# Kernel optimization log

Measured on AMD Instinct MI355X. Metric: run time of the kernel, lower is better.

## Reference

```python
import jax, jax.numpy as jnp
import numpy as np

B, L, D, N = 2, 2048, 1024, 16
DT_MIN, DT_MAX = 1e-3, 1e-1


def setup_inputs() -> dict:
    key = jax.random.key(0)
    ks = jax.random.split(key, 8)
    u = jax.random.normal(ks[0], (B, L, D), dtype=jnp.float32)
    # torch.nn.Linear weights are (out_features, in_features)
    W_dt = jax.random.normal(ks[1], (D, D), dtype=jnp.float32) * 0.02
    b_dt = jnp.zeros((D,), dtype=jnp.float32)
    W_B = jax.random.normal(ks[2], (D * N, D), dtype=jnp.float32) * 0.02
    b_B = jnp.zeros((D * N,), dtype=jnp.float32)
    W_C = jax.random.normal(ks[3], (D * N, D), dtype=jnp.float32) * 0.02
    b_C = jnp.zeros((D * N,), dtype=jnp.float32)
    # log_A init: log(1..N) broadcast over channels (HiPPO-ish diagonal)
    log_A = jnp.broadcast_to(jnp.log(jnp.arange(1, N + 1, dtype=jnp.float32)), (D, N))
    D_skip = jnp.ones((D,), dtype=jnp.float32)
    lo, hi = float(np.log(DT_MIN)), float(np.log(DT_MAX))
    dt_bias = jax.random.uniform(ks[4], (D,), dtype=jnp.float32) * (hi - lo) + lo
    return {"u": u, "log_A": log_A, "D_skip": D_skip, "dt_bias": dt_bias,
            "W_dt": W_dt, "b_dt": b_dt, "W_B": W_B, "b_B": b_B,
            "W_C": W_C, "b_C": b_C}


def reference(u, log_A, D_skip, dt_bias, W_dt, b_dt, W_B, b_B, W_C, b_C):
    b, l, d = u.shape
    n = log_A.shape[1]
    A = -jnp.exp(log_A)                                   # (d, n), A < 0
    # token-dependent parameters, computed for all timesteps at once
    dt = jax.nn.softplus(u @ W_dt.T + b_dt + dt_bias)     # (b, l, d)
    Bt = (u @ W_B.T + b_B).reshape(b, l, d, n)            # (b, l, d, n)
    Ct = (u @ W_C.T + b_C).reshape(b, l, d, n)            # (b, l, d, n)
    # exact ZOH discretisation
    A_bar = jnp.exp(dt[..., None] * A)                    # (b, l, d, n)
    B_bar = (A_bar - 1.0) / A * Bt                        # (b, l, d, n)
    x_in = B_bar * u[..., None]                           # (b, l, d, n)
    # recurrent scan over time
    def step(h, inp):
        a_t, x_t, c_t = inp                               # each (b, d, n)
        h = a_t * h + x_t
        y_t = jnp.sum(c_t * h, axis=-1)                   # (b, d)
        return h, y_t
    h0 = jnp.zeros((b, d, n), dtype=u.dtype)
    xs = (jnp.moveaxis(A_bar, 1, 0), jnp.moveaxis(x_in, 1, 0), jnp.moveaxis(Ct, 1, 0))
    _, ys = jax.lax.scan(step, h0, xs)                    # ys: (l, b, d)
    y = jnp.moveaxis(ys, 0, 1) + D_skip * u               # (b, l, d)
    return y
```

## Files before the change

### kernel.cpp

```cpp
#include <hip/hip_runtime.h>
#include <hip/hip_bf16.h>
#include <stdint.h>

constexpr int Bb = 2;
constexpr int Ll = 2048;
constexpr int Dd = 1024;
constexpr int Nn = 16;
constexpr int NB = Dd * Nn;
constexpr int SL = 64;
constexpr int NCH = Bb * Dd;
constexpr int KCAT = 3 * Dd;

typedef __bf16 bf16_t;
typedef __bf16 bf16x8 __attribute__((ext_vector_type(8)));
typedef __bf16 bf16x4 __attribute__((ext_vector_type(4)));
typedef float f32x4 __attribute__((ext_vector_type(4)));

__device__ inline void gld_lds16(const void* g, void* l) {
    __builtin_amdgcn_global_load_lds(
        (const __attribute__((address_space(1))) unsigned int*)g,
        (__attribute__((address_space(3))) unsigned int*)l, 16, 0, 0);
}

__global__ __launch_bounds__(256) void cvt_bf16(const float* __restrict__ s,
                                                bf16_t* __restrict__ d, int n4) {
    int i = blockIdx.x * 256 + threadIdx.x;
    const int stride = gridDim.x * 256;
    const float4* s4 = (const float4*)s;
    bf16x4* d4 = (bf16x4*)d;
    for (; i < n4; i += stride) {
        float4 v = s4[i];
        bf16x4 o = {(bf16_t)v.x, (bf16_t)v.y, (bf16_t)v.z, (bf16_t)v.w};
        d4[i] = o;
    }
}

__global__ __launch_bounds__(256) void build_ucat(const float* __restrict__ u,
                                                  bf16_t* __restrict__ ucat) {
    const int i = blockIdx.x * 256 + threadIdx.x;
    const int row = i >> 8;
    const int c = (i & 255) << 2;
    float4 v = ((const float4*)u)[i];
    bf16x4 hi = {(bf16_t)v.x, (bf16_t)v.y, (bf16_t)v.z, (bf16_t)v.w};
    bf16x4 lo = {(bf16_t)(v.x - (float)hi.x), (bf16_t)(v.y - (float)hi.y),
                 (bf16_t)(v.z - (float)hi.z), (bf16_t)(v.w - (float)hi.w)};
    bf16_t* r = ucat + (size_t)row * KCAT;
    *(bf16x4*)(r + c) = hi;
    *(bf16x4*)(r + Dd + c) = lo;
    *(bf16x4*)(r + 2 * Dd + c) = hi;
}

__global__ __launch_bounds__(256) void build_wcat(const float* __restrict__ w,
                                                  bf16_t* __restrict__ wcat) {
    const int i = blockIdx.x * 256 + threadIdx.x;
    const int row = i >> 8;
    const int c = (i & 255) << 2;
    float4 v = ((const float4*)w)[i];
    bf16x4 hi = {(bf16_t)v.x, (bf16_t)v.y, (bf16_t)v.z, (bf16_t)v.w};
    bf16x4 lo = {(bf16_t)(v.x - (float)hi.x), (bf16_t)(v.y - (float)hi.y),
                 (bf16_t)(v.z - (float)hi.z), (bf16_t)(v.w - (float)hi.w)};
    bf16_t* r = wcat + (size_t)row * KCAT;
    *(bf16x4*)(r + c) = hi;
    *(bf16x4*)(r + Dd + c) = hi;
    *(bf16x4*)(r + 2 * Dd + c) = lo;
}

template <int EP, typename OutT>
__global__ __launch_bounds__(256) void gemm_mfma(
    const bf16_t* __restrict__ Abase, int CL, int l0, int K,
    const bf16_t* __restrict__ W, const float* __restrict__ b1,
    const float* __restrict__ b2, OutT* __restrict__ C, int N)
{
    __shared__ bf16_t As[128 * 32];
    __shared__ bf16_t Bs[128 * 32];

    const int tid = threadIdx.x;
    const int bn = blockIdx.x * 128;
    const int rglob = blockIdx.y * 128;
    const int batch = rglob / CL;
    const int rin = rglob % CL;
    const bf16_t* Ap = Abase + ((size_t)batch * Ll + l0 + rin) * K;
    const bf16_t* Wp = W + (size_t)bn * K;
    OutT* Cp = C + (size_t)rglob * N;

    const int sr = tid >> 2;
    const int sc = (tid & 3) << 3;
    char* ldsA = (char*)As + tid * 16;
    char* ldsB = (char*)Bs + tid * 16;

    const int lane = tid & 63;
    const int wid = tid >> 6;
    const int wm = (wid & 1) << 6;
    const int wn = (wid >> 1) << 6;
    const int lr = lane & 15;
    const int lq = lane >> 4;

    f32x4 acc[4][4] = {};

    for (int k0 = 0; k0 < K; k0 += 32) {
        __syncthreads();
        gld_lds16(Ap + (size_t)sr * K + k0 + sc, ldsA);
        gld_lds16(Ap + (size_t)(sr + 64) * K + k0 + sc, ldsA + 4096);
        gld_lds16(Wp + (size_t)sr * K + k0 + sc, ldsB);
        gld_lds16(Wp + (size_t)(sr + 64) * K + k0 + sc, ldsB + 4096);
        __syncthreads();

        bf16x8 af[4], bfr[4];
#pragma unroll
        for (int mi = 0; mi < 4; ++mi)
            af[mi] = *(const bf16x8*)&As[(wm + mi * 16 + lr) * 32 + lq * 8];
#pragma unroll
        for (int ni = 0; ni < 4; ++ni)
            bfr[ni] = *(const bf16x8*)&Bs[(wn + ni * 16 + lr) * 32 + lq * 8];
#pragma unroll
        for (int mi = 0; mi < 4; ++mi)
#pragma unroll
            for (int ni = 0; ni < 4; ++ni)
                acc[mi][ni] = __builtin_amdgcn_mfma_f32_16x16x32_bf16(
                    af[mi], bfr[ni], acc[mi][ni], 0, 0, 0);
    }

#pragma unroll
    for (int ni = 0; ni < 4; ++ni) {
        const int col = bn + wn + ni * 16 + lr;
        const float bc = b1[col] + (EP == 1 ? b2[col] : 0.f);
#pragma unroll
        for (int mi = 0; mi < 4; ++mi)
#pragma unroll
            for (int i = 0; i < 4; ++i) {
                float v = acc[mi][ni][i] + bc;
                if (EP == 1) v = (v > 20.f) ? v : log1pf(__expf(v));
                Cp[(size_t)(wm + mi * 16 + lq * 4 + i) * N + col] = (OutT)v;
            }
    }
}

__global__ __launch_bounds__(256) void gemm_dt(
    const bf16_t* __restrict__ A, int K, const bf16_t* __restrict__ W,
    const float* __restrict__ b1, const float* __restrict__ b2,
    float* __restrict__ C)
{
    __shared__ bf16_t As[128 * 32];
    __shared__ bf16_t Bs[64 * 32];

    const int tid = threadIdx.x;
    const int bn = blockIdx.x * 64;
    const int row0 = blockIdx.y * 128;
    const bf16_t* Ap = A + (size_t)row0 * K;
    const bf16_t* Wp = W + (size_t)bn * K;
    float* Cp = C + (size_t)row0 * Dd;

    const int sr = tid >> 2;
    const int sc = (tid & 3) << 3;
    char* ldsA = (char*)As + tid * 16;
    char* ldsB = (char*)Bs + tid * 16;

    const int lane = tid & 63;
    const int wid = tid >> 6;
    const int wm = (wid & 1) << 6;
    const int wn = (wid >> 1) << 5;
    const int lr = lane & 15;
    const int lq = lane >> 4;

    f32x4 acc[4][2] = {};

    for (int k0 = 0; k0 < K; k0 += 32) {
        __syncthreads();
        gld_lds16(Ap + (size_t)sr * K + k0 + sc, ldsA);
        gld_lds16(Ap + (size_t)(sr + 64) * K + k0 + sc, ldsA + 4096);
        gld_lds16(Wp + (size_t)sr * K + k0 + sc, ldsB);
        __syncthreads();

        bf16x8 af[4], bfr[2];
#pragma unroll
        for (int mi = 0; mi < 4; ++mi)
            af[mi] = *(const bf16x8*)&As[(wm + mi * 16 + lr) * 32 + lq * 8];
#pragma unroll
        for (int ni = 0; ni < 2; ++ni)
            bfr[ni] = *(const bf16x8*)&Bs[(wn + ni * 16 + lr) * 32 + lq * 8];
#pragma unroll
        for (int mi = 0; mi < 4; ++mi)
#pragma unroll
            for (int ni = 0; ni < 2; ++ni)
                acc[mi][ni] = __builtin_amdgcn_mfma_f32_16x16x32_bf16(
                    bfr[ni], af[mi], acc[mi][ni], 0, 0, 0);
    }

#pragma unroll
    for (int ni = 0; ni < 2; ++ni) {
        const int col = bn + wn + ni * 16 + lq * 4;
        const float4 ba = *(const float4*)&b1[col];
        const float4 bb = *(const float4*)&b2[col];
        const float bc[4] = {ba.x + bb.x, ba.y + bb.y, ba.z + bb.z, ba.w + bb.w};
#pragma unroll
        for (int mi = 0; mi < 4; ++mi) {
            const int row = wm + mi * 16 + lr;
            f32x4 v;
#pragma unroll
            for (int i = 0; i < 4; ++i) {
                float t = acc[mi][ni][i] + bc[i];
                v[i] = (t > 20.f) ? t : log1pf(__expf(t));
            }
            *(f32x4*)(Cp + (size_t)row * Dd + col) = v;
        }
    }
}

__global__ __launch_bounds__(512, 2) void gemm256_bc(
    const bf16_t* __restrict__ Abase, int CL, int l0, int K,
    const bf16_t* __restrict__ WB, const bf16_t* __restrict__ WC,
    const float* __restrict__ bB, const float* __restrict__ bC,
    bf16_t* __restrict__ OB, bf16_t* __restrict__ OC)
{
    extern __shared__ char smem[];
    const int tid = threadIdx.x;

    const int NY = (2 * CL) >> 8;
    const int id = blockIdx.x;
    const int cx = id & 7;
    const int jj = id >> 3;
    const int x = cx * 16 + jj / NY;
    const int yb = jj % NY;

    const int rglob = yb * 256;
    const int batch = rglob / CL;
    const int rin = rglob % CL;
    const bf16_t* Ap = Abase + ((size_t)batch * Ll + l0 + rin) * K;

    const bf16_t* Wp; const float* bias; bf16_t* Co; int bn;
    if (x < 64) { Wp = WB; bias = bB; Co = OB; bn = x * 256; }
    else        { Wp = WC; bias = bC; Co = OC; bn = (x - 64) * 256; }
    Wp += (size_t)bn * K;
    bf16_t* Cp = Co + (size_t)rglob * NB;

    const int lane = tid & 63;
    const int wid = tid >> 6;
    const int wr = wid >> 2;
    const int wc = wid & 3;
    const int lr = lane & 15;
    const int lq = lane >> 4;
    const int NT = K >> 6;

    const int c0 = tid, c1 = tid + 512;
    const int r0 = c0 >> 3, r1 = c1 >> 3;
    const int kb0 = ((c0 & 7) << 3) ^ ((r0 & 7) << 3);
    const int kb1 = ((c1 & 7) << 3) ^ ((r1 & 7) << 3);

    auto stage = [&](const bf16_t* src, char* dst, int tt, int h) {
        gld_lds16(src + (size_t)(h * 128 + r0) * K + tt * 64 + kb0,
                  dst + h * 16384 + c0 * 16);
        gld_lds16(src + (size_t)(h * 128 + r1) * K + tt * 64 + kb1,
                  dst + h * 16384 + c1 * 16);
    };

    stage(Ap, smem, 0, 0);
    stage(Ap, smem, 0, 1);
    stage(Wp, smem + 32768, 0, 0);
    stage(Wp, smem + 32768, 0, 1);
    if (NT > 1) {
        stage(Wp, smem + 65536 + 32768, 1, 0);
        stage(Wp, smem + 65536 + 32768, 1, 1);
        asm volatile("s_waitcnt vmcnt(4)" ::: "memory");
    } else {
        asm volatile("s_waitcnt vmcnt(0)" ::: "memory");
    }
    __builtin_amdgcn_s_barrier();

    f32x4 acc[8][4] = {};
    const int xsw = (lr & 7) << 4;

    for (int t = 0; t < NT; ++t) {
        char* Ard = smem + ((t & 1) ? 65536 : 0);
        char* Brd = Ard + 32768;
        char* Awr = smem + ((t & 1) ? 0 : 65536);
        char* Bwr = Brd;

        bf16x8 bfr[2][4];
#pragma unroll
        for (int p = 0; p < 4; ++p) {
            if (p == 0) { if (t + 1 < NT) stage(Ap, Awr, t + 1, 0); }
            if (p == 1) { if (t + 1 < NT) stage(Ap, Awr, t + 1, 1); }
            if (p == 2) { if (t + 2 < NT) stage(Wp, Bwr, t + 2, 0); }
            if (p == 3) { if (t + 2 < NT) stage(Wp, Bwr, t + 2, 1); }

            if (p == 0) {
#pragma unroll
                for (int ks = 0; ks < 2; ++ks)
#pragma unroll
                    for (int ni = 0; ni < 4; ++ni)
                        bfr[ks][ni] = *(const bf16x8*)(Brd +
                            (wc * 64 + ni * 16 + lr) * 128 +
                            ((ks * 64 + lq * 16) ^ xsw));
            }
            bf16x8 a0k0 = *(const bf16x8*)(Ard +
                (wr * 128 + (2 * p) * 16 + lr) * 128 + ((lq * 16) ^ xsw));
            bf16x8 a0k1 = *(const bf16x8*)(Ard +
                (wr * 128 + (2 * p) * 16 + lr) * 128 + ((64 + lq * 16) ^ xsw));
            bf16x8 a1k0 = *(const bf16x8*)(Ard +
                (wr * 128 + (2 * p + 1) * 16 + lr) * 128 + ((lq * 16) ^ xsw));
            bf16x8 a1k1 = *(const bf16x8*)(Ard +
                (wr * 128 + (2 * p + 1) * 16 + lr) * 128 + ((64 + lq * 16) ^ xsw));

            __builtin_amdgcn_s_barrier();
            __builtin_amdgcn_s_setprio(1);
#pragma unroll
            for (int ni = 0; ni < 4; ++ni) {
                acc[2 * p][ni] = __builtin_amdgcn_mfma_f32_16x16x32_bf16(
                    bfr[0][ni], a0k0, acc[2 * p][ni], 0, 0, 0);
                acc[2 * p][ni] = __builtin_amdgcn_mfma_f32_16x16x32_bf16(
                    bfr[1][ni], a0k1, acc[2 * p][ni], 0, 0, 0);
                acc[2 * p + 1][ni] = __builtin_amdgcn_mfma_f32_16x16x32_bf16(
                    bfr[0][ni], a1k0, acc[2 * p + 1][ni], 0, 0, 0);
                acc[2 * p + 1][ni] = __builtin_amdgcn_mfma_f32_16x16x32_bf16(
                    bfr[1][ni], a1k1, acc[2 * p + 1][ni], 0, 0, 0);
            }
            __builtin_amdgcn_s_setprio(0);
            if (p == 3) {
                if (t + 2 < NT)
                    asm volatile("s_waitcnt vmcnt(4)" ::: "memory");
                else if (t + 1 < NT)
                    asm volatile("s_waitcnt vmcnt(0)" ::: "memory");
            }
            __builtin_amdgcn_s_barrier();
        }
    }

    float4 bv[4];
#pragma unroll
    for (int ni = 0; ni < 4; ++ni)
        bv[ni] = *(const float4*)&bias[bn + wc * 64 + ni * 16 + lq * 4];
#pragma unroll
    for (int mi = 0; mi < 8; ++mi) {
        const size_t rowoff = (size_t)(wr * 128 + mi * 16 + lr) * NB;
#pragma unroll
        for (int ni = 0; ni < 4; ++ni) {
            const int col = bn + wc * 64 + ni * 16 + lq * 4;
            bf16x4 o = {(bf16_t)(acc[mi][ni][0] + bv[ni].x),
                        (bf16_t)(acc[mi][ni][1] + bv[ni].y),
                        (bf16_t)(acc[mi][ni][2] + bv[ni].z),
                        (bf16_t)(acc[mi][ni][3] + bv[ni].w)};
            *(bf16x4*)(Cp + rowoff + col) = o;
        }
    }
}

__global__ __launch_bounds__(256) void scan_seg_local(
    const float* __restrict__ u, const float* __restrict__ dt,
    const bf16_t* __restrict__ Bt_c, const float* __restrict__ log_A,
    float* __restrict__ pseg, float* __restrict__ hseg, int CL, int l0)
{
    const int tid = threadIdx.x;
    const int g = tid >> 4, n = tid & 15;
    const int gid = blockIdx.x * 16 + g;
    const int ch = gid & (NCH - 1);
    const int s = gid >> 11;
    const int b = ch >> 10, d = ch & (Dd - 1);

    const float A = -__expf(log_A[d * Nn + n]);
    const float rA = 1.f / A;

    size_t idx_bn = (size_t)(b * CL + s * SL) * NB + d * Nn + n;
    size_t idx_u = ((size_t)b * Ll + l0 + s * SL) * Dd + d;

    float p = 1.f, h = 0.f;
    for (int l = 0; l < SL; ++l) {
        const float dtv = dt[idx_u];
        const float uv = u[idx_u];
        const float bv = (float)Bt_c[idx_bn];
        const float a = __expf(dtv * A);
        p *= a;
        h = a * h + (a - 1.f) * rA * bv * uv;
        idx_bn += NB; idx_u += Dd;
    }
    const size_t o = ((size_t)s * NCH + ch) * Nn + n;
    pseg[o] = p;
    hseg[o] = h;
}

__global__ __launch_bounds__(256) void scan_combine(
    const float* __restrict__ pseg, const float* __restrict__ hseg,
    float* __restrict__ hin_arr, float* __restrict__ h_state,
    int NSEG, int l0)
{
    const int t = blockIdx.x * 256 + threadIdx.x;
    float hin = (l0 == 0) ? 0.f : h_state[t];
    for (int s = 0; s < NSEG; ++s) {
        const size_t o = (size_t)s * (NCH * Nn) + t;
        hin_arr[o] = hin;
        hin = pseg[o] * hin + hseg[o];
    }
    h_state[t] = hin;
}

__global__ __launch_bounds__(256) void scan_seg_final(
    const float* __restrict__ u, const float* __restrict__ dt,
    const bf16_t* __restrict__ Bt_c, const bf16_t* __restrict__ Ct_c,
    const float* __restrict__ log_A, const float* __restrict__ D_skip,
    const float* __restrict__ hin_arr, float* __restrict__ y, int CL, int l0)
{
    const int tid = threadIdx.x;
    const int g = tid >> 4, n = tid & 15;
    const int gid = blockIdx.x * 16 + g;
    const int ch = gid & (NCH - 1);
    const int s = gid >> 11;
    const int b = ch >> 10, d = ch & (Dd - 1);

    const float A = -__expf(log_A[d * Nn + n]);
    const float rA = 1.f / A;
    const float Dsk = D_skip[d];

    size_t idx_bn = (size_t)(b * CL + s * SL) * NB + d * Nn + n;
    size_t idx_u = ((size_t)b * Ll + l0 + s * SL) * Dd + d;

    float h = hin_arr[((size_t)s * NCH + ch) * Nn + n];
    for (int l = 0; l < SL; ++l) {
        const float dtv = dt[idx_u];
        const float uv = u[idx_u];
        const float bv = (float)Bt_c[idx_bn];
        const float cv = (float)Ct_c[idx_bn];
        const float a = __expf(dtv * A);
        h = a * h + (a - 1.f) * rA * bv * uv;
        float p = cv * h;
        p += __shfl_xor(p, 1);
        p += __shfl_xor(p, 2);
        p += __shfl_xor(p, 4);
        p += __shfl_xor(p, 8);
        if (n == 0) y[idx_u] = p + Dsk * uv;
        idx_bn += NB; idx_u += Dd;
    }
}

static inline size_t al256(size_t x) { return (x + 255) & ~(size_t)255; }

extern "C" void kernel_launch(void* const* d_in, const int* in_sizes, int n_in,
                              void* d_out, int out_size, void* d_ws, size_t ws_size,
                              hipStream_t stream) {
    const float* u       = (const float*)d_in[0];
    const float* log_A   = (const float*)d_in[1];
    const float* D_skip  = (const float*)d_in[2];
    const float* dt_bias = (const float*)d_in[3];
    const float* W_dt    = (const float*)d_in[4];
    const float* b_dt    = (const float*)d_in[5];
    const float* W_B     = (const float*)d_in[6];
    const float* b_B     = (const float*)d_in[7];
    const float* W_C     = (const float*)d_in[8];
    const float* b_C     = (const float*)d_in[9];
    float* y = (float*)d_out;

    hipFuncSetAttribute(reinterpret_cast<const void*>(gemm256_bc),
                        hipFuncAttributeMaxDynamicSharedMemorySize, 131072);

    const size_t sz_ubf  = al256((size_t)Bb * Ll * Dd * 2);
    const size_t sz_w    = al256((size_t)NB * Dd * 2);
    const size_t sz_h    = al256((size_t)NCH * Nn * 4);
    const size_t sz_dtf  = al256((size_t)Bb * Ll * Dd * 4);
    const size_t sz_ucat = al256((size_t)Bb * Ll * KCAT * 2);
    const size_t sz_wcat = al256((size_t)Dd * KCAT * 2);

    int CL = 128;
    const int cands[5] = {2048, 1024, 512, 256, 128};
    for (int i = 0; i < 5; ++i) {
        const int c = cands[i];
        const int nseg = c / SL;
        const size_t seg = 3 * al256((size_t)nseg * NCH * Nn * 4);
        const size_t chunk = 2 * al256((size_t)2 * c * NB * 2);
        const size_t ovl = sz_ucat + sz_wcat;
        const size_t need = sz_ubf + 2 * sz_w + sz_h + sz_dtf + seg +
                            (chunk > ovl ? chunk : ovl);
        if (need <= ws_size) { CL = c; break; }
    }
    const int NSEG = CL / SL;

    char* p = (char*)d_ws;
    bf16_t* u_bf   = (bf16_t*)p; p += sz_ubf;
    bf16_t* wB_bf  = (bf16_t*)p; p += sz_w;
    bf16_t* wC_bf  = (bf16_t*)p; p += sz_w;
    float* h_state = (float*)p; p += sz_h;
    float* dt_full = (float*)p; p += sz_dtf;
    const size_t sz_seg1 = al256((size_t)NSEG * NCH * Nn * 4);
    float* pseg    = (float*)p; p += sz_seg1;
    float* hseg    = (float*)p; p += sz_seg1;
    float* hin_arr = (float*)p; p += sz_seg1;
    char* chunk0 = p;
    bf16_t* Bt_c = (bf16_t*)chunk0;
    bf16_t* Ct_c = (bf16_t*)(chunk0 + al256((size_t)2 * CL * NB * 2));
    bf16_t* u_cat = (bf16_t*)chunk0;
    bf16_t* w_cat = (bf16_t*)(chunk0 + sz_ucat);

    cvt_bf16<<<2048, 256, 0, stream>>>(u, u_bf, Bb * Ll * Dd / 4);
    cvt_bf16<<<2048, 256, 0, stream>>>(W_B, wB_bf, NB * Dd / 4);
    cvt_bf16<<<2048, 256, 0, stream>>>(W_C, wC_bf, NB * Dd / 4);
    build_ucat<<<Bb * Ll * Dd / 4 / 256, 256, 0, stream>>>(u, u_cat);
    build_wcat<<<Dd * Dd / 4 / 256, 256, 0, stream>>>(W_dt, w_cat);

    gemm_dt<<<dim3(Dd / 64, Bb * Ll / 128), 256, 0, stream>>>(
        u_cat, KCAT, w_cat, b_dt, dt_bias, dt_full);

    const bool use256 = (CL % 256 == 0);
    for (int l0 = 0; l0 < Ll; l0 += CL) {
        if (use256) {
            const int NY = 2 * CL / 256;
            gemm256_bc<<<dim3(128 * NY), 512, 131072, stream>>>(
                u_bf, CL, l0, Dd, wB_bf, wC_bf, b_B, b_C, Bt_c, Ct_c);
        } else {
            gemm_mfma<0, bf16_t><<<dim3(NB / 128, 2 * CL / 128), 256, 0, stream>>>(
                u_bf, CL, l0, Dd, wB_bf, b_B, nullptr, Bt_c, NB);
            gemm_mfma<0, bf16_t><<<dim3(NB / 128, 2 * CL / 128), 256, 0, stream>>>(
                u_bf, CL, l0, Dd, wC_bf, b_C, nullptr, Ct_c, NB);
        }
        scan_seg_local<<<dim3(128 * NSEG), 256, 0, stream>>>(
            u, dt_full, Bt_c, log_A, pseg, hseg, CL, l0);
        scan_combine<<<dim3(128), 256, 0, stream>>>(
            pseg, hseg, hin_arr, h_state, NSEG, l0);
        scan_seg_final<<<dim3(128 * NSEG), 256, 0, stream>>>(
            u, dt_full, Bt_c, Ct_c, log_A, D_skip, hin_arr, y, CL, l0);
    }
}
```

Measured before the change: 689.1 us.

## Shrink B/C GEMM tile to 256x128 with triple-buffered weights for higher occupancy

```diff
diff --git a/kernel.cpp b/kernel.cpp
--- a/kernel.cpp
+++ b/kernel.cpp
@@ -36,7 +36,8 @@
 }
 
 __global__ __launch_bounds__(256) void build_ucat(const float* __restrict__ u,
-                                                  bf16_t* __restrict__ ucat) {
+                                                  bf16_t* __restrict__ ucat,
+                                                  bf16_t* __restrict__ ubf) {
     const int i = blockIdx.x * 256 + threadIdx.x;
     const int row = i >> 8;
     const int c = (i & 255) << 2;
@@ -48,6 +49,7 @@
     *(bf16x4*)(r + c) = hi;
     *(bf16x4*)(r + Dd + c) = lo;
     *(bf16x4*)(r + 2 * Dd + c) = hi;
+    *(bf16x4*)(ubf + (size_t)i * 4) = hi;
 }
 
 __global__ __launch_bounds__(256) void build_wcat(const float* __restrict__ w,
@@ -206,7 +208,7 @@
     }
 }
 
-__global__ __launch_bounds__(512, 2) void gemm256_bc(
+__global__ __launch_bounds__(512, 4) void gemm256_bc(
     const bf16_t* __restrict__ Abase, int CL, int l0, int K,
     const bf16_t* __restrict__ WB, const bf16_t* __restrict__ WC,
     const float* __restrict__ bB, const float* __restrict__ bC,
@@ -219,7 +221,8 @@
     const int id = blockIdx.x;
     const int cx = id & 7;
     const int jj = id >> 3;
-    const int x = cx * 16 + jj / NY;
+    const int xs_per = (gridDim.x >> 3) / NY;
+    const int x = cx * xs_per + jj / NY;
     const int yb = jj % NY;
 
     const int rglob = yb * 256;
@@ -228,101 +231,80 @@
     const bf16_t* Ap = Abase + ((size_t)batch * Ll + l0 + rin) * K;
 
     const bf16_t* Wp; const float* bias; bf16_t* Co; int bn;
-    if (x < 64) { Wp = WB; bias = bB; Co = OB; bn = x * 256; }
-    else        { Wp = WC; bias = bC; Co = OC; bn = (x - 64) * 256; }
+    if (x < 128) { Wp = WB; bias = bB; Co = OB; bn = x * 128; }
+    else         { Wp = WC; bias = bC; Co = OC; bn = (x - 128) * 128; }
     Wp += (size_t)bn * K;
     bf16_t* Cp = Co + (size_t)rglob * NB;
 
     const int lane = tid & 63;
     const int wid = tid >> 6;
-    const int wr = wid >> 2;
-    const int wc = wid & 3;
+    const int wr = wid >> 1;
+    const int wc = wid & 1;
     const int lr = lane & 15;
     const int lq = lane >> 4;
-    const int NT = K >> 6;
-
-    const int c0 = tid, c1 = tid + 512;
-    const int r0 = c0 >> 3, r1 = c1 >> 3;
-    const int kb0 = ((c0 & 7) << 3) ^ ((r0 & 7) << 3);
-    const int kb1 = ((c1 & 7) << 3) ^ ((r1 & 7) << 3);
-
-    auto stage = [&](const bf16_t* src, char* dst, int tt, int h) {
-        gld_lds16(src + (size_t)(h * 128 + r0) * K + tt * 64 + kb0,
-                  dst + h * 16384 + c0 * 16);
-        gld_lds16(src + (size_t)(h * 128 + r1) * K + tt * 64 + kb1,
-                  dst + h * 16384 + c1 * 16);
+    const int NT = K >> 5;
+
+    const int r0 = tid >> 2;
+    const int ksrc = (((tid & 3) ^ ((r0 >> 1) & 3)) << 3);
+
+    auto stageA = [&](int tt, int h) {
+        gld_lds16(Ap + (size_t)(h * 128 + r0) * K + tt * 32 + ksrc,
+                  smem + (tt & 1) * 16384 + h * 8192 + tid * 16);
     };
-
-    stage(Ap, smem, 0, 0);
-    stage(Ap, smem, 0, 1);
-    stage(Wp, smem + 32768, 0, 0);
-    stage(Wp, smem + 32768, 0, 1);
+    auto stageB = [&](int tt, int slot) {
+        gld_lds16(Wp + (size_t)r0 * K + tt * 32 + ksrc,
+                  smem + 32768 + slot * 8192 + tid * 16);
+    };
+
+    stageA(0, 0); stageA(0, 1);
+    stageB(0, 0);
     if (NT > 1) {
-        stage(Wp, smem + 65536 + 32768, 1, 0);
-        stage(Wp, smem + 65536 + 32768, 1, 1);
-        asm volatile("s_waitcnt vmcnt(4)" ::: "memory");
+        stageB(1, 1);
+        asm volatile("s_waitcnt vmcnt(1)" ::: "memory");
     } else {
         asm volatile("s_waitcnt vmcnt(0)" ::: "memory");
     }
     __builtin_amdgcn_s_barrier();
 
-    f32x4 acc[8][4] = {};
-    const int xsw = (lr & 7) << 4;
+    f32x4 acc[4][4] = {};
+    const int lqx = (lq << 4) ^ (((lr >> 1) & 3) << 4);
+    int bR = 0;
 
     for (int t = 0; t < NT; ++t) {
-        char* Ard = smem + ((t & 1) ? 65536 : 0);
-        char* Brd = Ard + 32768;
-        char* Awr = smem + ((t & 1) ? 0 : 65536);
-        char* Bwr = Brd;
-
-        bf16x8 bfr[2][4];
-#pragma unroll
-        for (int p = 0; p < 4; ++p) {
-            if (p == 0) { if (t + 1 < NT) stage(Ap, Awr, t + 1, 0); }
-            if (p == 1) { if (t + 1 < NT) stage(Ap, Awr, t + 1, 1); }
-            if (p == 2) { if (t + 2 < NT) stage(Wp, Bwr, t + 2, 0); }
-            if (p == 3) { if (t + 2 < NT) stage(Wp, Bwr, t + 2, 1); }
-
-            if (p == 0) {
-#pragma unroll
-                for (int ks = 0; ks < 2; ++ks)
-#pragma unroll
-                    for (int ni = 0; ni < 4; ++ni)
-                        bfr[ks][ni] = *(const bf16x8*)(Brd +
-                            (wc * 64 + ni * 16 + lr) * 128 +
-                            ((ks * 64 + lq * 16) ^ xsw));
-            }
-            bf16x8 a0k0 = *(const bf16x8*)(Ard +
-                (wr * 128 + (2 * p) * 16 + lr) * 128 + ((lq * 16) ^ xsw));
-            bf16x8 a0k1 = *(const bf16x8*)(Ard +
-                (wr * 128 + (2 * p) * 16 + lr) * 128 + ((64 + lq * 16) ^ xsw));
-            bf16x8 a1k0 = *(const bf16x8*)(Ard +
-                (wr * 128 + (2 * p + 1) * 16 + lr) * 128 + ((lq * 16) ^ xsw));
-            bf16x8 a1k1 = *(const bf16x8*)(Ard +
-                (wr * 128 + (2 * p + 1) * 16 + lr) * 128 + ((64 + lq * 16) ^ xsw));
-
-            __builtin_amdgcn_s_barrier();
-            __builtin_amdgcn_s_setprio(1);
-#pragma unroll
-            for (int ni = 0; ni < 4; ++ni) {
-                acc[2 * p][ni] = __builtin_amdgcn_mfma_f32_16x16x32_bf16(
-                    bfr[0][ni], a0k0, acc[2 * p][ni], 0, 0, 0);
-                acc[2 * p][ni] = __builtin_amdgcn_mfma_f32_16x16x32_bf16(
-                    bfr[1][ni], a0k1, acc[2 * p][ni], 0, 0, 0);
-                acc[2 * p + 1][ni] = __builtin_amdgcn_mfma_f32_16x16x32_bf16(
-                    bfr[0][ni], a1k0, acc[2 * p + 1][ni], 0, 0, 0);
-                acc[2 * p + 1][ni] = __builtin_amdgcn_mfma_f32_16x16x32_bf16(
-                    bfr[1][ni], a1k1, acc[2 * p + 1][ni], 0, 0, 0);
-            }
-            __builtin_amdgcn_s_setprio(0);
-            if (p == 3) {
-                if (t + 2 < NT)
-                    asm volatile("s_waitcnt vmcnt(4)" ::: "memory");
-                else if (t + 1 < NT)
-                    asm volatile("s_waitcnt vmcnt(0)" ::: "memory");
-            }
-            __builtin_amdgcn_s_barrier();
+        if (t + 1 < NT) { stageA(t + 1, 0); stageA(t + 1, 1); }
+        int bS = bR + 2; if (bS >= 3) bS -= 3;
+        if (t + 2 < NT) stageB(t + 2, bS);
+
+        const char* Ard = smem + (t & 1) * 16384;
+        const char* Brd = smem + 32768 + bR * 8192;
+        bf16x8 afr[4], bfr[4];
+#pragma unroll
+        for (int mi = 0; mi < 4; ++mi) {
+            const int row = wr * 64 + mi * 16 + lr;
+            afr[mi] = *(const bf16x8*)(Ard + (row >> 7) * 8192 +
+                                       (row & 127) * 64 + lqx);
         }
+#pragma unroll
+        for (int ni = 0; ni < 4; ++ni) {
+            const int row = wc * 64 + ni * 16 + lr;
+            bfr[ni] = *(const bf16x8*)(Brd + row * 64 + lqx);
+        }
+
+        __builtin_amdgcn_s_barrier();
+        __builtin_amdgcn_s_setprio(1);
+#pragma unroll
+        for (int mi = 0; mi < 4; ++mi)
+#pragma unroll
+            for (int ni = 0; ni < 4; ++ni)
+                acc[mi][ni] = __builtin_amdgcn_mfma_f32_16x16x32_bf16(
+                    bfr[ni], afr[mi], acc[mi][ni], 0, 0, 0);
+        __builtin_amdgcn_s_setprio(0);
+        if (t + 2 < NT)
+            asm volatile("s_waitcnt vmcnt(1)" ::: "memory");
+        else if (t + 1 < NT)
+            asm volatile("s_waitcnt vmcnt(0)" ::: "memory");
+        __builtin_amdgcn_s_barrier();
+        bR = bR + 1; if (bR >= 3) bR -= 3;
     }
 
     float4 bv[4];
@@ -330,8 +312,8 @@
     for (int ni = 0; ni < 4; ++ni)
         bv[ni] = *(const float4*)&bias[bn + wc * 64 + ni * 16 + lq * 4];
 #pragma unroll
-    for (int mi = 0; mi < 8; ++mi) {
-        const size_t rowoff = (size_t)(wr * 128 + mi * 16 + lr) * NB;
+    for (int mi = 0; mi < 4; ++mi) {
+        const size_t rowoff = (size_t)(wr * 64 + mi * 16 + lr) * NB;
 #pragma unroll
         for (int ni = 0; ni < 4; ++ni) {
             const int col = bn + wc * 64 + ni * 16 + lq * 4;
@@ -448,7 +430,7 @@
     float* y = (float*)d_out;
 
     hipFuncSetAttribute(reinterpret_cast<const void*>(gemm256_bc),
-                        hipFuncAttributeMaxDynamicSharedMemorySize, 131072);
+                        hipFuncAttributeMaxDynamicSharedMemorySize, 57344);
 
     const size_t sz_ubf  = al256((size_t)Bb * Ll * Dd * 2);
     const size_t sz_w    = al256((size_t)NB * Dd * 2);
@@ -487,10 +469,9 @@
     bf16_t* u_cat = (bf16_t*)chunk0;
     bf16_t* w_cat = (bf16_t*)(chunk0 + sz_ucat);
 
-    cvt_bf16<<<2048, 256, 0, stream>>>(u, u_bf, Bb * Ll * Dd / 4);
     cvt_bf16<<<2048, 256, 0, stream>>>(W_B, wB_bf, NB * Dd / 4);
     cvt_bf16<<<2048, 256, 0, stream>>>(W_C, wC_bf, NB * Dd / 4);
-    build_ucat<<<Bb * Ll * Dd / 4 / 256, 256, 0, stream>>>(u, u_cat);
+    build_ucat<<<Bb * Ll * Dd / 4 / 256, 256, 0, stream>>>(u, u_cat, u_bf);
     build_wcat<<<Dd * Dd / 4 / 256, 256, 0, stream>>>(W_dt, w_cat);
 
     gemm_dt<<<dim3(Dd / 64, Bb * Ll / 128), 256, 0, stream>>>(
@@ -500,7 +481,7 @@
     for (int l0 = 0; l0 < Ll; l0 += CL) {
         if (use256) {
             const int NY = 2 * CL / 256;
-            gemm256_bc<<<dim3(128 * NY), 512, 131072, stream>>>(
+            gemm256_bc<<<dim3(256 * NY), 512, 57344, stream>>>(
                 u_bf, CL, l0, Dd, wB_bf, wC_bf, b_B, b_C, Bt_c, Ct_c);
         } else {
             gemm_mfma<0, bf16_t><<<dim3(NB / 128, 2 * CL / 128), 256, 0, stream>>>(
```

Result: slower. 719.0 us (+4.3%).

## Deepen GEMM prefetch pipelines and fold u bf16 conversion into build_ucat

Applied to the files above, without the earlier changes.

```diff
diff --git a/kernel.cpp b/kernel.cpp
--- a/kernel.cpp
+++ b/kernel.cpp
@@ -36,7 +36,8 @@
 }
 
 __global__ __launch_bounds__(256) void build_ucat(const float* __restrict__ u,
-                                                  bf16_t* __restrict__ ucat) {
+                                                  bf16_t* __restrict__ ucat,
+                                                  bf16_t* __restrict__ ubf) {
     const int i = blockIdx.x * 256 + threadIdx.x;
     const int row = i >> 8;
     const int c = (i & 255) << 2;
@@ -48,6 +49,7 @@
     *(bf16x4*)(r + c) = hi;
     *(bf16x4*)(r + Dd + c) = lo;
     *(bf16x4*)(r + 2 * Dd + c) = hi;
+    *(bf16x4*)(ubf + (size_t)i * 4) = hi;
 }
 
 __global__ __launch_bounds__(256) void build_wcat(const float* __restrict__ w,
@@ -135,71 +137,111 @@
     }
 }
 
-__global__ __launch_bounds__(256) void gemm_dt(
+__global__ __launch_bounds__(512, 4) void gemm_dt(
     const bf16_t* __restrict__ A, int K, const bf16_t* __restrict__ W,
     const float* __restrict__ b1, const float* __restrict__ b2,
     float* __restrict__ C)
 {
-    __shared__ bf16_t As[128 * 32];
-    __shared__ bf16_t Bs[64 * 32];
-
+    extern __shared__ char smem[];
+    char* const smA = smem;
+    char* const smB = smem + 49152;
     const int tid = threadIdx.x;
-    const int bn = blockIdx.x * 64;
+    const int bn = blockIdx.x * 128;
     const int row0 = blockIdx.y * 128;
     const bf16_t* Ap = A + (size_t)row0 * K;
     const bf16_t* Wp = W + (size_t)bn * K;
     float* Cp = C + (size_t)row0 * Dd;
 
-    const int sr = tid >> 2;
-    const int sc = (tid & 3) << 3;
-    char* ldsA = (char*)As + tid * 16;
-    char* ldsB = (char*)Bs + tid * 16;
-
     const int lane = tid & 63;
     const int wid = tid >> 6;
-    const int wm = (wid & 1) << 6;
-    const int wn = (wid >> 1) << 5;
+    const int wr = wid >> 2;
+    const int wc = wid & 3;
     const int lr = lane & 15;
     const int lq = lane >> 4;
+    const int NT = K >> 6;
+
+    const int c0 = tid, c1 = tid + 512;
+    const int r0 = c0 >> 3, r1 = c1 >> 3;
+    const int kb0 = ((c0 & 7) << 3) ^ ((r0 & 7) << 3);
+    const int kb1 = ((c1 & 7) << 3) ^ ((r1 & 7) << 3);
+
+    auto stageA = [&](int tt, int slot) {
+        gld_lds16(Ap + (size_t)r0 * K + tt * 64 + kb0, smA + slot * 16384 + c0 * 16);
+        gld_lds16(Ap + (size_t)r1 * K + tt * 64 + kb1, smA + slot * 16384 + c1 * 16);
+    };
+    auto stageB = [&](int tt, int slot) {
+        gld_lds16(Wp + (size_t)r0 * K + tt * 64 + kb0, smB + slot * 16384 + c0 * 16);
+        gld_lds16(Wp + (size_t)r1 * K + tt * 64 + kb1, smB + slot * 16384 + c1 * 16);
+    };
+
+    stageA(0, 0); stageB(0, 0); stageA(1, 1); stageB(1, 1);
+    asm volatile("s_waitcnt vmcnt(4)" ::: "memory");
+    __builtin_amdgcn_s_barrier();
 
     f32x4 acc[4][2] = {};
-
-    for (int k0 = 0; k0 < K; k0 += 32) {
-        __syncthreads();
-        gld_lds16(Ap + (size_t)sr * K + k0 + sc, ldsA);
-        gld_lds16(Ap + (size_t)(sr + 64) * K + k0 + sc, ldsA + 4096);
-        gld_lds16(Wp + (size_t)sr * K + k0 + sc, ldsB);
-        __syncthreads();
-
-        bf16x8 af[4], bfr[2];
-#pragma unroll
-        for (int mi = 0; mi < 4; ++mi)
-            af[mi] = *(const bf16x8*)&As[(wm + mi * 16 + lr) * 32 + lq * 8];
-#pragma unroll
-        for (int ni = 0; ni < 2; ++ni)
-            bfr[ni] = *(const bf16x8*)&Bs[(wn + ni * 16 + lr) * 32 + lq * 8];
-#pragma unroll
-        for (int mi = 0; mi < 4; ++mi)
-#pragma unroll
-            for (int ni = 0; ni < 2; ++ni)
-                acc[mi][ni] = __builtin_amdgcn_mfma_f32_16x16x32_bf16(
-                    bfr[ni], af[mi], acc[mi][ni], 0, 0, 0);
+    const int xsw = (lr & 7) << 4;
+    int as_rd = 0, as_wr = 2;
+
+    for (int t = 0; t < NT; ++t) {
+        const char* Ard = smA + as_rd * 16384;
+        const char* Brd = smB + (t & 1) * 16384;
+
+        bf16x8 bfr[2][2];
+#pragma unroll
+        for (int p = 0; p < 4; ++p) {
+            if (p == 0 && t + 2 < NT) stageA(t + 2, as_wr);
+            if (p == 2 && t + 2 < NT) stageB(t + 2, (t & 1));
+
+            if (p == 0) {
+#pragma unroll
+                for (int ks = 0; ks < 2; ++ks)
+#pragma unroll
+                    for (int ni = 0; ni < 2; ++ni)
+                        bfr[ks][ni] = *(const bf16x8*)(Brd +
+                            (wc * 32 + ni * 16 + lr) * 128 +
+                            ((ks * 64 + lq * 16) ^ xsw));
+            }
+            bf16x8 ak0 = *(const bf16x8*)(Ard +
+                (wr * 64 + p * 16 + lr) * 128 + ((lq * 16) ^ xsw));
+            bf16x8 ak1 = *(const bf16x8*)(Ard +
+                (wr * 64 + p * 16 + lr) * 128 + ((64 + lq * 16) ^ xsw));
+
+            __builtin_amdgcn_s_barrier();
+            __builtin_amdgcn_s_setprio(1);
+#pragma unroll
+            for (int ni = 0; ni < 2; ++ni) {
+                acc[p][ni] = __builtin_amdgcn_mfma_f32_16x16x32_bf16(
+                    bfr[0][ni], ak0, acc[p][ni], 0, 0, 0);
+                acc[p][ni] = __builtin_amdgcn_mfma_f32_16x16x32_bf16(
+                    bfr[1][ni], ak1, acc[p][ni], 0, 0, 0);
+            }
+            __builtin_amdgcn_s_setprio(0);
+            if (p == 3) {
+                if (t + 2 < NT)
+                    asm volatile("s_waitcnt vmcnt(4)" ::: "memory");
+                else if (t + 1 < NT)
+                    asm volatile("s_waitcnt vmcnt(0)" ::: "memory");
+            }
+            __builtin_amdgcn_s_barrier();
+        }
+        ++as_rd; if (as_rd == 3) as_rd = 0;
+        ++as_wr; if (as_wr == 3) as_wr = 0;
     }
 
 #pragma unroll
     for (int ni = 0; ni < 2; ++ni) {
-        const int col = bn + wn + ni * 16 + lq * 4;
+        const int col = bn + wc * 32 + ni * 16 + lq * 4;
         const float4 ba = *(const float4*)&b1[col];
         const float4 bb = *(const float4*)&b2[col];
         const float bc[4] = {ba.x + bb.x, ba.y + bb.y, ba.z + bb.z, ba.w + bb.w};
 #pragma unroll
         for (int mi = 0; mi < 4; ++mi) {
-            const int row = wm + mi * 16 + lr;
+            const int row = wr * 64 + mi * 16 + lr;
             f32x4 v;
 #pragma unroll
             for (int i = 0; i < 4; ++i) {
-                float t = acc[mi][ni][i] + bc[i];
-                v[i] = (t > 20.f) ? t : log1pf(__expf(t));
+                float tv = acc[mi][ni][i] + bc[i];
+                v[i] = (tv > 20.f) ? tv : log1pf(__expf(tv));
             }
             *(f32x4*)(Cp + (size_t)row * Dd + col) = v;
         }
@@ -213,6 +255,8 @@
     bf16_t* __restrict__ OB, bf16_t* __restrict__ OC)
 {
     extern __shared__ char smem[];
+    char* const smA = smem;
+    char* const smB = smem + 98304;
     const int tid = threadIdx.x;
 
     const int NY = (2 * CL) >> 8;
@@ -246,42 +290,41 @@
     const int kb0 = ((c0 & 7) << 3) ^ ((r0 & 7) << 3);
     const int kb1 = ((c1 & 7) << 3) ^ ((r1 & 7) << 3);
 
-    auto stage = [&](const bf16_t* src, char* dst, int tt, int h) {
-        gld_lds16(src + (size_t)(h * 128 + r0) * K + tt * 64 + kb0,
-                  dst + h * 16384 + c0 * 16);
-        gld_lds16(src + (size_t)(h * 128 + r1) * K + tt * 64 + kb1,
-                  dst + h * 16384 + c1 * 16);
+    auto stageA = [&](int tt, int slot, int h) {
+        gld_lds16(Ap + (size_t)(h * 128 + r0) * K + tt * 64 + kb0,
+                  smA + slot * 32768 + h * 16384 + c0 * 16);
+        gld_lds16(Ap + (size_t)(h * 128 + r1) * K + tt * 64 + kb1,
+                  smA + slot * 32768 + h * 16384 + c1 * 16);
     };
-
-    stage(Ap, smem, 0, 0);
-    stage(Ap, smem, 0, 1);
-    stage(Wp, smem + 32768, 0, 0);
-    stage(Wp, smem + 32768, 0, 1);
-    if (NT > 1) {
-        stage(Wp, smem + 65536 + 32768, 1, 0);
-        stage(Wp, smem + 65536 + 32768, 1, 1);
-        asm volatile("s_waitcnt vmcnt(4)" ::: "memory");
-    } else {
-        asm volatile("s_waitcnt vmcnt(0)" ::: "memory");
-    }
+    auto stageB = [&](int tt, int slot, int h) {
+        gld_lds16(Wp + (size_t)(h * 128 + r0) * K + tt * 64 + kb0,
+                  smB + slot * 32768 + h * 16384 + c0 * 16);
+        gld_lds16(Wp + (size_t)(h * 128 + r1) * K + tt * 64 + kb1,
+                  smB + slot * 32768 + h * 16384 + c1 * 16);
+    };
+
+    stageA(0, 0, 0); stageA(0, 0, 1);
+    stageB(0, 0, 0); stageB(0, 0, 1);
+    stageA(1, 1, 0); stageA(1, 1, 1);
+    stageB(1, 1, 0); stageB(1, 1, 1);
+    asm volatile("s_waitcnt vmcnt(8)" ::: "memory");
     __builtin_amdgcn_s_barrier();
 
     f32x4 acc[8][4] = {};
     const int xsw = (lr & 7) << 4;
+    int as_rd = 0, as_wr = 2;
 
     for (int t = 0; t < NT; ++t) {
-        char* Ard = smem + ((t & 1) ? 65536 : 0);
-        char* Brd = Ard + 32768;
-        char* Awr = smem + ((t & 1) ? 0 : 65536);
-        char* Bwr = Brd;
+        const char* Ard = smA + as_rd * 32768;
+        const char* Brd = smB + (t & 1) * 32768;
 
         bf16x8 bfr[2][4];
 #pragma unroll
         for (int p = 0; p < 4; ++p) {
-            if (p == 0) { if (t + 1 < NT) stage(Ap, Awr, t + 1, 0); }
-            if (p == 1) { if (t + 1 < NT) stage(Ap, Awr, t + 1, 1); }
-            if (p == 2) { if (t + 2 < NT) stage(Wp, Bwr, t + 2, 0); }
-            if (p == 3) { if (t + 2 < NT) stage(Wp, Bwr, t + 2, 1); }
+            if (p == 0) { if (t + 2 < NT) stageA(t + 2, as_wr, 0); }
+            if (p == 1) { if (t + 2 < NT) stageA(t + 2, as_wr, 1); }
+            if (p == 2) { if (t + 2 < NT) stageB(t + 2, (t & 1), 0); }
+            if (p == 3) { if (t + 2 < NT) stageB(t + 2, (t & 1), 1); }
 
             if (p == 0) {
 #pragma unroll
@@ -317,12 +360,14 @@
             __builtin_amdgcn_s_setprio(0);
             if (p == 3) {
                 if (t + 2 < NT)
-                    asm volatile("s_waitcnt vmcnt(4)" ::: "memory");
+                    asm volatile("s_waitcnt vmcnt(8)" ::: "memory");
                 else if (t + 1 < NT)
                     asm volatile("s_waitcnt vmcnt(0)" ::: "memory");
             }
             __builtin_amdgcn_s_barrier();
         }
+        ++as_rd; if (as_rd == 3) as_rd = 0;
+        ++as_wr; if (as_wr == 3) as_wr = 0;
     }
 
     float4 bv[4];
@@ -448,7 +493,9 @@
     float* y = (float*)d_out;
 
     hipFuncSetAttribute(reinterpret_cast<const void*>(gemm256_bc),
-                        hipFuncAttributeMaxDynamicSharedMemorySize, 131072);
+                        hipFuncAttributeMaxDynamicSharedMemorySize, 163840);
+    hipFuncSetAttribute(reinterpret_cast<const void*>(gemm_dt),
+                        hipFuncAttributeMaxDynamicSharedMemorySize, 81920);
 
     const size_t sz_ubf  = al256((size_t)Bb * Ll * Dd * 2);
     const size_t sz_w    = al256((size_t)NB * Dd * 2);
@@ -487,20 +534,19 @@
     bf16_t* u_cat = (bf16_t*)chunk0;
     bf16_t* w_cat = (bf16_t*)(chunk0 + sz_ucat);
 
-    cvt_bf16<<<2048, 256, 0, stream>>>(u, u_bf, Bb * Ll * Dd / 4);
     cvt_bf16<<<2048, 256, 0, stream>>>(W_B, wB_bf, NB * Dd / 4);
     cvt_bf16<<<2048, 256, 0, stream>>>(W_C, wC_bf, NB * Dd / 4);
-    build_ucat<<<Bb * Ll * Dd / 4 / 256, 256, 0, stream>>>(u, u_cat);
+    build_ucat<<<Bb * Ll * Dd / 4 / 256, 256, 0, stream>>>(u, u_cat, u_bf);
     build_wcat<<<Dd * Dd / 4 / 256, 256, 0, stream>>>(W_dt, w_cat);
 
-    gemm_dt<<<dim3(Dd / 64, Bb * Ll / 128), 256, 0, stream>>>(
+    gemm_dt<<<dim3(Dd / 128, Bb * Ll / 128), 512, 81920, stream>>>(
         u_cat, KCAT, w_cat, b_dt, dt_bias, dt_full);
 
     const bool use256 = (CL % 256 == 0);
     for (int l0 = 0; l0 < Ll; l0 += CL) {
         if (use256) {
             const int NY = 2 * CL / 256;
-            gemm256_bc<<<dim3(128 * NY), 512, 131072, stream>>>(
+            gemm256_bc<<<dim3(128 * NY), 512, 163840, stream>>>(
                 u_bf, CL, l0, Dd, wB_bf, wC_bf, b_B, b_C, Bt_c, Ct_c);
         } else {
             gemm_mfma<0, bf16_t><<<dim3(NB / 128, 2 * CL / 128), 256, 0, stream>>>(
```

After: 672.3 us. 1.02x faster.
